# Performance work log

Measured on AMD Instinct MI355X. Metric: run time of the kernel, lower is better.

Reference implementation:

```python
import jax, jax.numpy as jnp
import numpy as np

N = 262144          # anchors per batch (dense detector)
C = 80              # COCO classes; targets==C means background/negative
ALPHA = 0.25
GAMMA = 2.0
LOSS_WEIGHT = 1.0
MAX_SCHEMA = 65536  # schema ints kept < 2**16 so float32 holds them exactly


def setup_inputs() -> dict:
    key = jax.random.key(0)
    k1, k2, k3 = jax.random.split(key, 3)
    pred = jax.random.normal(k1, (N, C), dtype=jnp.float32)
    targets = jax.random.randint(k2, (N,), 0, C + 1, dtype=jnp.int32)
    weight = jax.random.randint(k3, (N,), 0, MAX_SCHEMA, dtype=jnp.int32).astype(jnp.float32)
    return {"pred": pred, "targets": targets, "weight": weight}


def reference(pred, targets, weight):
    num_classes = pred.shape[1]
    # --- vectorized cross_mask: bit-unpack schema for negative rows ---
    # cur_schema (reversed binary string) => bit c of int(schema)
    wint = weight.astype(jnp.int32)
    bits = ((wint[:, None] >> jnp.arange(num_classes, dtype=jnp.int32)[None, :]) & 1).astype(pred.dtype)  # (N,C)
    neg = (targets == num_classes)[:, None]                       # (N,1) negative rows
    cross_mask = jnp.where(neg, bits, jnp.ones((), pred.dtype))   # (N,C)
    # --- sigmoid focal loss (mmcv semantics: target==c is positive; target==C -> all-zero one-hot) ---
    onehot = jax.nn.one_hot(targets, num_classes, dtype=pred.dtype)  # (N,C); bg row is all zeros
    p = jax.nn.sigmoid(pred)
    pt = onehot * (1.0 - p) + (1.0 - onehot) * p
    focal_w = (ALPHA * onehot + (1.0 - ALPHA) * (1.0 - onehot)) * pt ** GAMMA
    # stable BCE-with-logits: -log sigmoid(x) = softplus(-x)
    bce = onehot * jax.nn.softplus(-pred) + (1.0 - onehot) * jax.nn.softplus(pred)
    # use_weight=True: weight binarized to {0,1} per row
    w = jnp.where(weight > 0, 1.0, 0.0).astype(pred.dtype)[:, None]
    loss = focal_w * bce * w * cross_mask
    return LOSS_WEIGHT * loss.mean()
```

## Files before the change

kernel.cpp:

```cpp
#include <hip/hip_runtime.h>
#include <hip/hip_bf16.h>


#define NCLS 80
#define C4   (NCLS / 4)
#define NBLOCKS 4096
#define NTHREADS 256
#define STRIDE (NBLOCKS * NTHREADS)

typedef float f32x4 __attribute__((ext_vector_type(4)));

__device__ __forceinline__ float log1p_poly(float x) {
    float p = -0.0064535442f;
    p = __builtin_fmaf(p, x,  0.0360884937f);
    p = __builtin_fmaf(p, x, -0.0953293897f);
    p = __builtin_fmaf(p, x,  0.1676540711f);
    p = __builtin_fmaf(p, x, -0.2407338084f);
    p = __builtin_fmaf(p, x,  0.3317990258f);
    p = __builtin_fmaf(p, x, -0.4998741238f);
    p = __builtin_fmaf(p, x,  0.9999964239f);
    return p * x;
}

__device__ __forceinline__ float elem_term(float x, int c, int t, int wi, bool neg) {
    const bool  pos = (c == t);
    const int   bit = (c < 32) ? ((wi >> c) & 1) : 0;
    const float m   = neg ? (float)bit : 1.0f;
    const float a   = pos ? 0.25f : 0.75f;
    const float y   = pos ? -x : x;
    const float e   = __expf(-fabsf(x));
    const float inv = __builtin_amdgcn_rcpf(1.0f + e);
    const float s   = (y >= 0.0f) ? inv : e * inv;
    const float sp  = fmaxf(y, 0.0f) + log1p_poly(e);
    return (a * m) * (s * s) * sp;
}

template<int KITERS>
__global__ void __launch_bounds__(NTHREADS, 8)
cfs_main(const float* __restrict__ pred,
         const int*   __restrict__ targets,
         const float* __restrict__ weight,
         float* __restrict__ partials,
         int total4) {
    const int tid = blockIdx.x * NTHREADS + threadIdx.x;

    float acc = 0.0f;
    if constexpr (KITERS > 0) {
        f32x4 x[KITERS];
        int   tt[KITERS];
        float wf[KITERS];
        #pragma unroll
        for (int k = 0; k < KITERS; ++k) {
            const int i = tid + k * STRIDE;
            const int n = i / C4;
            x[k]  = reinterpret_cast<const f32x4*>(pred)[i];
            tt[k] = targets[n];
            wf[k] = weight[n];
        }
        #pragma unroll
        for (int k = 0; k < KITERS; ++k) {
            const int i  = tid + k * STRIDE;
            const int n  = i / C4;
            const int c0 = (i - n * C4) * 4;
            const int   t   = tt[k];
            const float w   = wf[k];
            const int   wi  = (int)w;
            const bool  neg = (t == NCLS);
            const float rw  = (w > 0.0f) ? 1.0f : 0.0f;
            const float s4 = elem_term(x[k][0], c0 + 0, t, wi, neg)
                           + elem_term(x[k][1], c0 + 1, t, wi, neg)
                           + elem_term(x[k][2], c0 + 2, t, wi, neg)
                           + elem_term(x[k][3], c0 + 3, t, wi, neg);
            acc = __builtin_fmaf(rw, s4, acc);
        }
    } else {
        for (int i = tid; i < total4; i += STRIDE) {
            const int n  = i / C4;
            const int c0 = (i - n * C4) * 4;
            const f32x4 x4 = reinterpret_cast<const f32x4*>(pred)[i];
            const int   t   = targets[n];
            const float w   = weight[n];
            const int   wi  = (int)w;
            const bool  neg = (t == NCLS);
            const float rw  = (w > 0.0f) ? 1.0f : 0.0f;
            const float s4 = elem_term(x4[0], c0 + 0, t, wi, neg)
                           + elem_term(x4[1], c0 + 1, t, wi, neg)
                           + elem_term(x4[2], c0 + 2, t, wi, neg)
                           + elem_term(x4[3], c0 + 3, t, wi, neg);
            acc = __builtin_fmaf(rw, s4, acc);
        }
    }

    #pragma unroll
    for (int off = 32; off > 0; off >>= 1)
        acc += __shfl_down(acc, off, 64);

    __shared__ float smem[NTHREADS / 64];
    const int lane = threadIdx.x & 63;
    const int wid  = threadIdx.x >> 6;
    if (lane == 0) smem[wid] = acc;
    __syncthreads();
    if (threadIdx.x == 0)
        partials[blockIdx.x] = smem[0] + smem[1] + smem[2] + smem[3];
}

__global__ void __launch_bounds__(NTHREADS)
cfs_reduce(const float* __restrict__ partials, float* __restrict__ out,
           int nparts4, float scale) {
    float acc = 0.0f;
    for (int i = threadIdx.x; i < nparts4; i += NTHREADS) {
        const f32x4 p4 = reinterpret_cast<const f32x4*>(partials)[i];
        acc += (p4[0] + p4[1]) + (p4[2] + p4[3]);
    }
    #pragma unroll
    for (int off = 32; off > 0; off >>= 1)
        acc += __shfl_down(acc, off, 64);

    __shared__ float smem[NTHREADS / 64];
    const int lane = threadIdx.x & 63;
    const int wid  = threadIdx.x >> 6;
    if (lane == 0) smem[wid] = acc;
    __syncthreads();
    if (threadIdx.x == 0)
        out[0] = (smem[0] + smem[1] + smem[2] + smem[3]) * scale;
}

extern "C" void kernel_launch(void* const* d_in, const int* in_sizes, int n_in,
                              void* d_out, int out_size, void* d_ws, size_t ws_size,
                              hipStream_t stream) {
    const float* pred     = (const float*)d_in[0];
    const int*   targets  = (const int*)  d_in[1];
    const float* weight   = (const float*)d_in[2];
    float*       out      = (float*)d_out;
    float*       partials = (float*)d_ws;

    const int n_rows = in_sizes[1];
    const int total4 = n_rows * C4;
    const float inv_total = 1.0f / (float)(n_rows * NCLS);

    if (total4 == 5 * STRIDE) {
        cfs_main<5><<<NBLOCKS, NTHREADS, 0, stream>>>(pred, targets, weight, partials, total4);
    } else {
        cfs_main<0><<<NBLOCKS, NTHREADS, 0, stream>>>(pred, targets, weight, partials, total4);
    }
    cfs_reduce<<<1, NTHREADS, 0, stream>>>(partials, out, NBLOCKS / 4, inv_total);
}
```

Before: 26.49 us.

## Rework focal term math with log2 softplus and hoist per-row masks

Replaces the polynomial log1p with a hardware log2 of (1+e), and computes the per-quad class mask and row weight factors once per quad instead of once per element. Grid size drops to 2560 blocks, each doing 8 iterations, and row indices advance by a fixed row step instead of a per-iteration division. The explicit load-all-then-compute staging and the occupancy hint in launch bounds are removed, so how many loads stay in flight now depends on the compiler. Fewer ALU ops per element should help if the kernel is compute-bound, at the cost of a slightly different accuracy profile for softplus.

```diff
diff --git a/kernel.cpp b/kernel.cpp
--- a/kernel.cpp
+++ b/kernel.cpp
@@ -4,39 +4,46 @@
 
 #define NCLS 80
 #define C4   (NCLS / 4)
-#define NBLOCKS 4096
+#define NBLOCKS 2560
 #define NTHREADS 256
+#define KIT 8
 #define STRIDE (NBLOCKS * NTHREADS)
+#define ROWSTEP (STRIDE / C4)
 
 typedef float f32x4 __attribute__((ext_vector_type(4)));
 
-__device__ __forceinline__ float log1p_poly(float x) {
-    float p = -0.0064535442f;
-    p = __builtin_fmaf(p, x,  0.0360884937f);
-    p = __builtin_fmaf(p, x, -0.0953293897f);
-    p = __builtin_fmaf(p, x,  0.1676540711f);
-    p = __builtin_fmaf(p, x, -0.2407338084f);
-    p = __builtin_fmaf(p, x,  0.3317990258f);
-    p = __builtin_fmaf(p, x, -0.4998741238f);
-    p = __builtin_fmaf(p, x,  0.9999964239f);
-    return p * x;
-}
-
-__device__ __forceinline__ float elem_term(float x, int c, int t, int wi, bool neg) {
-    const bool  pos = (c == t);
-    const int   bit = (c < 32) ? ((wi >> c) & 1) : 0;
-    const float m   = neg ? (float)bit : 1.0f;
-    const float a   = pos ? 0.25f : 0.75f;
-    const float y   = pos ? -x : x;
-    const float e   = __expf(-fabsf(x));
-    const float inv = __builtin_amdgcn_rcpf(1.0f + e);
-    const float s   = (y >= 0.0f) ? inv : e * inv;
-    const float sp  = fmaxf(y, 0.0f) + log1p_poly(e);
-    return (a * m) * (s * s) * sp;
+__device__ __forceinline__ float quad_term(f32x4 x4, int t, float w, int c0) {
+    const int   wi  = (int)w;
+    const bool  neg = (t == NCLS);
+    const float qn  = (w > 0.0f) ? 0.75f : 0.0f;
+    const float qp  = (w > 0.0f) ? 0.25f : 0.0f;
+    const int   wsh   = (c0 < 32) ? (wi >> c0) : 0;
+    const int   maskA = neg ? (wsh & 15) : 15;
+    float acc = 0.0f;
+    #pragma unroll
+    for (int j = 0; j < 4; ++j) {
+        const float x   = x4[j];
+        const float e   = __expf(-fabsf(x));
+        const float d   = 1.0f + e;
+        const float r   = __builtin_amdgcn_rcpf(d);
+        const float sB  = e * r;
+        const bool  f   = (x >= 0.0f);
+        const float s   = f ? r : sB;
+        const float s1  = f ? sB : r;
+        const float lg  = __log2f(d);
+        const float sp  = __builtin_fmaf(lg, 0.69314718055994531f, fmaxf(x, 0.0f));
+        const float sp1 = sp - x;
+        const float g   = (s * s) * sp;
+        const float g1  = (s1 * s1) * sp1;
+        const float cN  = ((maskA >> j) & 1) ? qn : 0.0f;
+        const bool  ist = ((c0 + j) == t);
+        acc += ist ? (qp * g1) : (cN * g);
+    }
+    return acc;
 }
 
 template<int KITERS>
-__global__ void __launch_bounds__(NTHREADS, 8)
+__global__ void __launch_bounds__(NTHREADS)
 cfs_main(const float* __restrict__ pred,
          const int*   __restrict__ targets,
          const float* __restrict__ weight,
@@ -46,48 +53,21 @@
 
     float acc = 0.0f;
     if constexpr (KITERS > 0) {
-        f32x4 x[KITERS];
-        int   tt[KITERS];
-        float wf[KITERS];
+        const int n0 = tid / C4;
+        const int c0 = (tid - n0 * C4) * 4;
         #pragma unroll
         for (int k = 0; k < KITERS; ++k) {
             const int i = tid + k * STRIDE;
-            const int n = i / C4;
-            x[k]  = reinterpret_cast<const f32x4*>(pred)[i];
-            tt[k] = targets[n];
-            wf[k] = weight[n];
-        }
-        #pragma unroll
-        for (int k = 0; k < KITERS; ++k) {
-            const int i  = tid + k * STRIDE;
-            const int n  = i / C4;
-            const int c0 = (i - n * C4) * 4;
-            const int   t   = tt[k];
-            const float w   = wf[k];
-            const int   wi  = (int)w;
-            const bool  neg = (t == NCLS);
-            const float rw  = (w > 0.0f) ? 1.0f : 0.0f;
-            const float s4 = elem_term(x[k][0], c0 + 0, t, wi, neg)
-                           + elem_term(x[k][1], c0 + 1, t, wi, neg)
-                           + elem_term(x[k][2], c0 + 2, t, wi, neg)
-                           + elem_term(x[k][3], c0 + 3, t, wi, neg);
-            acc = __builtin_fmaf(rw, s4, acc);
+            const int n = n0 + k * ROWSTEP;
+            const f32x4 x4 = reinterpret_cast<const f32x4*>(pred)[i];
+            acc += quad_term(x4, targets[n], weight[n], c0);
         }
     } else {
         for (int i = tid; i < total4; i += STRIDE) {
             const int n  = i / C4;
             const int c0 = (i - n * C4) * 4;
             const f32x4 x4 = reinterpret_cast<const f32x4*>(pred)[i];
-            const int   t   = targets[n];
-            const float w   = weight[n];
-            const int   wi  = (int)w;
-            const bool  neg = (t == NCLS);
-            const float rw  = (w > 0.0f) ? 1.0f : 0.0f;
-            const float s4 = elem_term(x4[0], c0 + 0, t, wi, neg)
-                           + elem_term(x4[1], c0 + 1, t, wi, neg)
-                           + elem_term(x4[2], c0 + 2, t, wi, neg)
-                           + elem_term(x4[3], c0 + 3, t, wi, neg);
-            acc = __builtin_fmaf(rw, s4, acc);
+            acc += quad_term(x4, targets[n], weight[n], c0);
         }
     }
 
@@ -138,8 +118,8 @@
     const int total4 = n_rows * C4;
     const float inv_total = 1.0f / (float)(n_rows * NCLS);
 
-    if (total4 == 5 * STRIDE) {
-        cfs_main<5><<<NBLOCKS, NTHREADS, 0, stream>>>(pred, targets, weight, partials, total4);
+    if (total4 == KIT * STRIDE) {
+        cfs_main<KIT><<<NBLOCKS, NTHREADS, 0, stream>>>(pred, targets, weight, partials, total4);
     } else {
         cfs_main<0><<<NBLOCKS, NTHREADS, 0, stream>>>(pred, targets, weight, partials, total4);
     }
```

Measured after the change: 26.39 us. No clear change (-0.4%).
